# Optimization experiments

Measured on AMD Instinct MI355X. Metric: run time of the kernel, lower is better.

The kernel has to match this reference:

```python
import jax, jax.numpy as jnp
import numpy as np

D = 1024
H = 16
HD = D // H
B = 2
S = 2048


def setup_inputs() -> dict:
    key = jax.random.key(0)
    ks = jax.random.split(key, 9)
    sc = 1.0 / np.sqrt(D)
    return {
        "x": jax.random.normal(ks[0], (B, S, D), dtype=jnp.float32),
        "attention_mask": jnp.ones((B, S), dtype=jnp.int32),
        "Wq": jax.random.normal(ks[1], (D, D), dtype=jnp.float32) * sc,
        "bq": jax.random.normal(ks[2], (D,), dtype=jnp.float32) * 0.02,
        "Wk": jax.random.normal(ks[3], (D, D), dtype=jnp.float32) * sc,
        "bk": jax.random.normal(ks[4], (D,), dtype=jnp.float32) * 0.02,
        "Wv": jax.random.normal(ks[5], (D, D), dtype=jnp.float32) * sc,
        "bv": jax.random.normal(ks[6], (D,), dtype=jnp.float32) * 0.02,
        "Wo": jax.random.normal(ks[7], (D, D), dtype=jnp.float32) * sc,
        "bo": jax.random.normal(ks[8], (D,), dtype=jnp.float32) * 0.02,
    }


def reference(x, attention_mask, Wq, bq, Wk, bk, Wv, bv, Wo, bo):
    Bb, Ss, d = x.shape
    # projections (torch Linear: x @ W.T + b; here W stored as [in,out])
    q = (x @ Wq + bq).reshape(Bb, Ss, H, HD).transpose(0, 2, 1, 3)  # [B,H,S,hd]
    k = (x @ Wk + bk).reshape(Bb, Ss, H, HD).transpose(0, 2, 1, 3)
    v = (x @ Wv + bv).reshape(Bb, Ss, H, HD).transpose(0, 2, 1, 3)
    dots = jnp.einsum("bhqd,bhkd->bhqk", q, k) / np.sqrt(HD)  # [B,H,S,S]
    causal = jnp.triu(jnp.ones((Ss, Ss), dtype=bool), k=1)  # True above diagonal
    dots = jnp.where(causal[None, None], -jnp.inf, dots)
    pad = (attention_mask == 0)[:, None, None, :]  # [B,1,1,S]
    dots = jnp.where(pad, -jnp.inf, dots)
    scores = jax.nn.softmax(dots, axis=-1)
    o = jnp.einsum("bhqk,bhkd->bhqd", scores, v)  # [B,H,S,hd]
    o = o.transpose(0, 2, 1, 3).reshape(Bb, Ss, d)
    return o @ Wo + bo
```

## Files before the change

### kernel.cpp

```cpp
#include <hip/hip_runtime.h>

#define D_  1024
#define H_  16
#define HD_ 64
#define B_  2
#define S_  2048
#define M_  (B_*S_)

typedef _Float16 f16;
typedef _Float16 f16x8 __attribute__((ext_vector_type(8)));
typedef _Float16 f16x4 __attribute__((ext_vector_type(4)));
typedef _Float16 f16x2 __attribute__((ext_vector_type(2)));
typedef float    f32x4 __attribute__((ext_vector_type(4)));

#define GLOAD_LDS16(g, l) \
  __builtin_amdgcn_global_load_lds((__attribute__((address_space(1))) const void*)(g), \
                                   (__attribute__((address_space(3))) void*)(l), 16, 0, 0)

__global__ void k_cvt_x(const float* __restrict__ x, f16* __restrict__ xb) {
  int i = blockIdx.x * blockDim.x + threadIdx.x;
  float4 v = ((const float4*)x)[i];
  f16x4 o = { (f16)v.x, (f16)v.y, (f16)v.z, (f16)v.w };
  ((f16x4*)xb)[i] = o;
}

__global__ void k_twt(const float* __restrict__ W, f16* __restrict__ WT) {
  __shared__ float t[32][33];
  int n0 = blockIdx.x * 32, k0 = blockIdx.y * 32;
  int tx = threadIdx.x, ty = threadIdx.y;
  #pragma unroll
  for (int i = 0; i < 4; i++)
    t[ty + i*8][tx] = W[(size_t)(k0 + ty + i*8) * D_ + n0 + tx];
  __syncthreads();
  #pragma unroll
  for (int i = 0; i < 4; i++)
    WT[(size_t)(n0 + ty + i*8) * D_ + k0 + tx] = (f16)t[tx][ty + i*8];
}

template<int MODE>
__device__ __forceinline__ void gemm_body(const f16* __restrict__ A,
                                          const f16* __restrict__ Bt,
                                          const float* __restrict__ bias,
                                          void* __restrict__ Cout) {
  __shared__ __align__(16) f16 lA[128 * 32];
  __shared__ __align__(16) f16 lB[128 * 32];
  const int tid = threadIdx.x;
  const int wv = tid >> 6, lane = tid & 63;
  const int m0 = blockIdx.y * 128, n0 = blockIdx.x * 128;
  const int fr = lane & 15, fg = lane >> 4;
  const int wm = wv >> 1, wn = wv & 1;
  f32x4 acc[4][4] = {};

  for (int k0 = 0; k0 < D_; k0 += 32) {
    #pragma unroll
    for (int it = 0; it < 2; ++it) {
      int c = wv + it * 4;
      int row = c * 16 + (lane >> 2);
      int kk = (lane & 3) * 8;
      GLOAD_LDS16(A  + (size_t)(m0 + row) * D_ + k0 + kk, lA + c * 512);
      GLOAD_LDS16(Bt + (size_t)(n0 + row) * D_ + k0 + kk, lB + c * 512);
    }
    __syncthreads();
    f16x8 a[4], b[4];
    #pragma unroll
    for (int i = 0; i < 4; i++) a[i] = *(const f16x8*)&lA[(wm*64 + i*16 + fr) * 32 + fg * 8];
    #pragma unroll
    for (int j = 0; j < 4; j++) b[j] = *(const f16x8*)&lB[(wn*64 + j*16 + fr) * 32 + fg * 8];
    #pragma unroll
    for (int i = 0; i < 4; i++)
      #pragma unroll
      for (int j = 0; j < 4; j++)
        acc[i][j] = __builtin_amdgcn_mfma_f32_16x16x32_f16(a[i], b[j], acc[i][j], 0, 0, 0);
    __syncthreads();
  }

  #pragma unroll
  for (int i = 0; i < 4; i++) {
    #pragma unroll
    for (int j = 0; j < 4; j++) {
      int grow0 = m0 + wm*64 + i*16 + fg*4;
      int gcol  = n0 + wn*64 + j*16 + fr;
      float bb = bias[gcol];
      #pragma unroll
      for (int r = 0; r < 4; r++) {
        float val = acc[i][j][r] + bb;
        int grow = grow0 + r;
        if (MODE == 0) {
          int b = grow >> 11, s = grow & (S_ - 1);
          int h = gcol >> 6,  hd = gcol & (HD_ - 1);
          ((f16*)Cout)[((size_t)(b * H_ + h) * S_ + s) * HD_ + hd] = (f16)val;
        } else {
          ((float*)Cout)[(size_t)grow * D_ + gcol] = val;
        }
      }
    }
  }
}

__global__ __launch_bounds__(256) void k_gemm_qkv(const f16* __restrict__ A,
                                                  const f16* __restrict__ WT0,
                                                  const float* __restrict__ bq,
                                                  const float* __restrict__ bk,
                                                  const float* __restrict__ bv,
                                                  f16* __restrict__ qkv) {
  int z = blockIdx.z;
  const f16* Bt = WT0 + (size_t)z * D_ * D_;
  const float* bias = (z == 0) ? bq : (z == 1) ? bk : bv;
  f16* outp = qkv + (size_t)z * M_ * D_;
  gemm_body<0>(A, Bt, bias, outp);
}

__global__ __launch_bounds__(256) void k_gemm_out(const f16* __restrict__ A,
                                                  const f16* __restrict__ Bt,
                                                  const float* __restrict__ bias,
                                                  float* __restrict__ Cout) {
  gemm_body<1>(A, Bt, bias, Cout);
}

#define POFF 8.65617025f

__global__ __launch_bounds__(256) void k_attn(const f16* __restrict__ Qh,
                                              const f16* __restrict__ Kh,
                                              const f16* __restrict__ Vh,
                                              const int* __restrict__ am,
                                              f16* __restrict__ O) {
  __shared__ __align__(16) f16 kt[2][64 * 64];
  __shared__ __align__(16) f16 vt[2][64 * 64];
  __shared__ __align__(16) f16 pl[4][16 * 64];

  const int tid = threadIdx.x;
  const int wv = tid >> 6, lane = tid & 63;
  const int fr = lane & 15, fg = lane >> 4;

  const int d = blockIdx.x;
  const int x = d & 7, j = d >> 3;
  const int bh = x + 8 * (j & 3);
  const int slot = j >> 2;
  const int b = bh >> 4, h = bh & 15;

  const f16* Qb = Qh + (size_t)bh * S_ * HD_;
  const f16* Kb = Kh + (size_t)bh * S_ * HD_;
  const f16* Vb = Vh + (size_t)bh * S_ * HD_;
  const int* amb = am + b * S_;
  f16* plw = pl[wv];

  const f16 qs = (f16)0.18033688f;
  const int ksrc = 8 * ((lane & 7) ^ (lane >> 3));
  const int swz = (fr & 7) << 3;
  const int vkk = (tid >> 3) * 2, vd0 = (tid & 7) * 8;
  const int vswz2 = (tid & 3) << 4;
  const f32x4 cinit = { -POFF, -POFF, -POFF, -POFF };

#define STAGE_K(t_, c_) do { \
    const f16* kp_ = Kb + (size_t)((t_) * 64) * HD_; \
    GLOAD_LDS16(kp_ + (size_t)((wv*2+0)*8 + (lane >> 3)) * HD_ + ksrc, &kt[c_][(wv*2+0)*512]); \
    GLOAD_LDS16(kp_ + (size_t)((wv*2+1)*8 + (lane >> 3)) * HD_ + ksrc, &kt[c_][(wv*2+1)*512]); \
  } while (0)

#define LOAD_V(t_) do { \
    const f16* vp_ = Vb + (size_t)((t_) * 64 + vkk) * HD_ + vd0; \
    vA = *(const f16x8*)vp_; vBr = *(const f16x8*)(vp_ + HD_); \
  } while (0)

#define WRITE_V(c_) do { \
    _Pragma("unroll") \
    for (int j_ = 0; j_ < 8; ++j_) { \
      f16x2 pr_ = { vA[j_], vBr[j_] }; \
      *(f16x2*)&vt[c_][(vd0 + j_) * 64 + ((vkk ^ (j_ << 3)) ^ vswz2)] = pr_; \
    } \
  } while (0)

  f16x8 vA, vBr;

  auto run_tile = [&](int qt, int nkb) {
    const int q0w = qt * 64 + wv * 16;

    f16x8 qf0, qf1;
    {
      f16x8 r0 = *(const f16x8*)&Qb[(size_t)(q0w + fr) * HD_ + fg*8];
      f16x8 r1 = *(const f16x8*)&Qb[(size_t)(q0w + fr) * HD_ + 32 + fg*8];
      qf0 = r0 * qs; qf1 = r1 * qs;
    }

    f32x4 accO[4] = {};
    float lrl = 0.f;

    STAGE_K(0, 0);
    LOAD_V(0);
    WRITE_V(0);
    __syncthreads();

    int c = 0;
    for (int t = 0; t < nkb; ++t) {
      const int kb = t * 64;
      const bool pre = (t + 1 < nkb);
      if (pre) { STAGE_K(t + 1, c ^ 1); LOAD_V(t + 1); }

      int4 a4[4];
      #pragma unroll
      for (int tt = 0; tt < 4; ++tt) a4[tt] = *(const int4*)&amb[kb + tt*16 + fg*4];

      const int dq = q0w - kb;
      int tm = (dq + 15) >> 4; if (tm > 3) tm = 3;
      const bool fullb = (dq >= 63);

      f32x4 s[4];
      #pragma unroll
      for (int tt = 0; tt < 4; ++tt) s[tt] = cinit;

      __builtin_amdgcn_s_setprio(1);
      #pragma unroll
      for (int tt = 0; tt < 4; ++tt) {
        if (tt <= tm) {
          const int kr = (tt*16 + fr) * 64;
          f16x8 kf0 = *(const f16x8*)&kt[c][kr + ((     fg*8) ^ swz)];
          f16x8 kf1 = *(const f16x8*)&kt[c][kr + ((32 + fg*8) ^ swz)];
          s[tt] = __builtin_amdgcn_mfma_f32_16x16x32_f16(kf0, qf0, s[tt], 0, 0, 0);
          s[tt] = __builtin_amdgcn_mfma_f32_16x16x32_f16(kf1, qf1, s[tt], 0, 0, 0);
        }
      }
      __builtin_amdgcn_s_setprio(0);

      const int thr = dq + fr;
      #pragma unroll
      for (int tt = 0; tt < 4; ++tt) {
        f16x4 pk4 = {};
        if (tt <= tm) {
          #pragma unroll
          for (int r = 0; r < 4; ++r) {
            float sv = s[tt][r];
            if (!fullb) sv = (tt*16 + fg*4 + r <= thr) ? sv : -1e30f;
            float p = exp2f(sv);
            int mr_ = (r == 0) ? a4[tt].x : (r == 1) ? a4[tt].y : (r == 2) ? a4[tt].z : a4[tt].w;
            p = mr_ ? p : 0.0f;
            lrl += p;
            pk4[r] = (f16)p;
          }
        }
        *(f16x4*)&plw[fr * 64 + ((tt*16 + fg*4) ^ swz)] = pk4;
      }

      __builtin_amdgcn_s_setprio(1);
      #pragma unroll
      for (int ks = 0; ks < 2; ++ks) {
        if (ks <= (tm >> 1)) {
          f16x8 pa = *(const f16x8*)&plw[fr * 64 + ((ks*32 + fg*8) ^ swz)];
          #pragma unroll
          for (int nt = 0; nt < 4; ++nt) {
            f16x8 vf = *(const f16x8*)&vt[c][(nt*16 + fr) * 64 +
                         ((ks*32 + fg*8) ^ swz ^ (((2*nt + (fr >> 3)) & 3) << 4))];
            accO[nt] = __builtin_amdgcn_mfma_f32_16x16x32_f16(pa, vf, accO[nt], 0, 0, 0);
          }
        }
      }
      __builtin_amdgcn_s_setprio(0);

      if (pre) WRITE_V(c ^ 1);
      __syncthreads();
      c ^= 1;
    }

    float v = lrl;
    v += __shfl_xor(v, 16);
    v += __shfl_xor(v, 32);
    float inv[4];
    #pragma unroll
    for (int r = 0; r < 4; ++r) {
      float sum = __shfl(v, (lane & 48) + 4 * ((lane >> 4) & 3) + r);
      inv[r] = __builtin_amdgcn_rcpf(sum);
    }
    #pragma unroll
    for (int nt = 0; nt < 4; ++nt) {
      int col = h * HD_ + nt*16 + fr;
      #pragma unroll
      for (int r = 0; r < 4; ++r) {
        int row = q0w + fg*4 + r;
        O[((size_t)b * S_ + row) * D_ + col] = (f16)(accO[nt][r] * inv[r]);
      }
    }
  };

  run_tile(slot, slot + 1);
  run_tile(31 - slot, 32 - slot);

#undef STAGE_K
#undef LOAD_V
#undef WRITE_V
}

extern "C" void kernel_launch(void* const* d_in, const int* in_sizes, int n_in,
                              void* d_out, int out_size, void* d_ws, size_t ws_size,
                              hipStream_t stream) {
  const float* x  = (const float*)d_in[0];
  const int*   am = (const int*)d_in[1];
  const float* Wq = (const float*)d_in[2];
  const float* bq = (const float*)d_in[3];
  const float* Wk = (const float*)d_in[4];
  const float* bk = (const float*)d_in[5];
  const float* Wv = (const float*)d_in[6];
  const float* bv = (const float*)d_in[7];
  const float* Wo = (const float*)d_in[8];
  const float* bo = (const float*)d_in[9];

  char* ws = (char*)d_ws;
  f16* xb  = (f16*)(ws);
  f16* wt  = (f16*)(ws + (8u  << 20));
  f16* qkv = (f16*)(ws + (16u << 20));
  f16* Ob  = (f16*)(ws + (40u << 20));

  k_cvt_x<<<4096, 256, 0, stream>>>(x, xb);

  dim3 tb(32, 8), tg(32, 32);
  k_twt<<<tg, tb, 0, stream>>>(Wq, wt + 0 * (size_t)(D_ * D_));
  k_twt<<<tg, tb, 0, stream>>>(Wk, wt + 1 * (size_t)(D_ * D_));
  k_twt<<<tg, tb, 0, stream>>>(Wv, wt + 2 * (size_t)(D_ * D_));
  k_twt<<<tg, tb, 0, stream>>>(Wo, wt + 3 * (size_t)(D_ * D_));

  k_gemm_qkv<<<dim3(8, 32, 3), 256, 0, stream>>>(xb, wt, bq, bk, bv, qkv);

  k_attn<<<dim3(512), 256, 0, stream>>>(qkv,
                                        qkv + (size_t)M_ * D_,
                                        qkv + 2 * (size_t)M_ * D_,
                                        am, Ob);

  k_gemm_out<<<dim3(8, 32), 256, 0, stream>>>(Ob, wt + 3 * (size_t)(D_ * D_), bo,
                                              (float*)d_out);
}
```

Baseline: 138.7 us.

## Split attention KV range across two blocks and combine partials in separate kernel

The attention kernel now launches twice as many blocks. Each block covers half of the key range for its pair of query tiles and writes unnormalized partial outputs plus row sums to workspace buffers. A new combine kernel adds the two partials, normalizes them, and writes the head-interleaved layout consumed by the output GEMM. A block-level check of whether the whole padding mask is valid also skips the per-element mask loads and selects when no keys are masked. The goal is more parallelism and better load balance on the GPU, at the cost of an extra kernel launch, extra global traffic and aliased workspace reuse.

Measured after the change: 139.3 us. Within noise of the previous version (+0.4%).

```diff
diff --git a/kernel.cpp b/kernel.cpp
--- a/kernel.cpp
+++ b/kernel.cpp
@@ -123,7 +123,8 @@
                                               const f16* __restrict__ Kh,
                                               const f16* __restrict__ Vh,
                                               const int* __restrict__ am,
-                                              f16* __restrict__ O) {
+                                              f16* __restrict__ OpA, f16* __restrict__ OpB,
+                                              float* __restrict__ lpA, float* __restrict__ lpB) {
   __shared__ __align__(16) f16 kt[2][64 * 64];
   __shared__ __align__(16) f16 vt[2][64 * 64];
   __shared__ __align__(16) f16 pl[4][16 * 64];
@@ -133,16 +134,33 @@
   const int fr = lane & 15, fg = lane >> 4;
 
   const int d = blockIdx.x;
-  const int x = d & 7, j = d >> 3;
-  const int bh = x + 8 * (j & 3);
-  const int slot = j >> 2;
+  const int lo = d & 255, kk4 = d >> 8;
+  const int bh = lo & 31;
+  const int m  = (lo >> 5) + 8 * (kk4 & 1);
+  const int typeB = kk4 >> 1;
   const int b = bh >> 4, h = bh & 15;
+  (void)h;
+
+  f16*   Op = typeB ? OpB : OpA;
+  float* lp = typeB ? lpB : lpA;
 
   const f16* Qb = Qh + (size_t)bh * S_ * HD_;
   const f16* Kb = Kh + (size_t)bh * S_ * HD_;
   const f16* Vb = Vh + (size_t)bh * S_ * HD_;
   const int* amb = am + b * S_;
   f16* plw = pl[wv];
+
+  volatile int* flag = (volatile int*)&pl[0][0];
+  if (tid == 0) *flag = 1;
+  __syncthreads();
+  {
+    int mv = 1;
+    #pragma unroll
+    for (int i = 0; i < 8; ++i) mv &= amb[tid * 8 + i];
+    if (!mv) *flag = 0;
+  }
+  __syncthreads();
+  const bool allv = (*flag != 0);
 
   const f16 qs = (f16)0.18033688f;
   const int ksrc = 8 * ((lane & 7) ^ (lane >> 3));
@@ -172,120 +190,158 @@
 
   f16x8 vA, vBr;
 
-  auto run_tile = [&](int qt, int nkb) {
+  auto run_half = [&](int qt, int t0, int t1) {
     const int q0w = qt * 64 + wv * 16;
-
-    f16x8 qf0, qf1;
-    {
-      f16x8 r0 = *(const f16x8*)&Qb[(size_t)(q0w + fr) * HD_ + fg*8];
-      f16x8 r1 = *(const f16x8*)&Qb[(size_t)(q0w + fr) * HD_ + 32 + fg*8];
-      qf0 = r0 * qs; qf1 = r1 * qs;
-    }
-
     f32x4 accO[4] = {};
     float lrl = 0.f;
 
-    STAGE_K(0, 0);
-    LOAD_V(0);
-    WRITE_V(0);
-    __syncthreads();
-
-    int c = 0;
-    for (int t = 0; t < nkb; ++t) {
-      const int kb = t * 64;
-      const bool pre = (t + 1 < nkb);
-      if (pre) { STAGE_K(t + 1, c ^ 1); LOAD_V(t + 1); }
-
-      int4 a4[4];
-      #pragma unroll
-      for (int tt = 0; tt < 4; ++tt) a4[tt] = *(const int4*)&amb[kb + tt*16 + fg*4];
-
-      const int dq = q0w - kb;
-      int tm = (dq + 15) >> 4; if (tm > 3) tm = 3;
-      const bool fullb = (dq >= 63);
-
-      f32x4 s[4];
-      #pragma unroll
-      for (int tt = 0; tt < 4; ++tt) s[tt] = cinit;
-
-      __builtin_amdgcn_s_setprio(1);
-      #pragma unroll
-      for (int tt = 0; tt < 4; ++tt) {
-        if (tt <= tm) {
-          const int kr = (tt*16 + fr) * 64;
-          f16x8 kf0 = *(const f16x8*)&kt[c][kr + ((     fg*8) ^ swz)];
-          f16x8 kf1 = *(const f16x8*)&kt[c][kr + ((32 + fg*8) ^ swz)];
-          s[tt] = __builtin_amdgcn_mfma_f32_16x16x32_f16(kf0, qf0, s[tt], 0, 0, 0);
-          s[tt] = __builtin_amdgcn_mfma_f32_16x16x32_f16(kf1, qf1, s[tt], 0, 0, 0);
-        }
+    if (t0 < t1) {
+      f16x8 qf0, qf1;
+      {
+        f16x8 r0 = *(const f16x8*)&Qb[(size_t)(q0w + fr) * HD_ + fg*8];
+        f16x8 r1 = *(const f16x8*)&Qb[(size_t)(q0w + fr) * HD_ + 32 + fg*8];
+        qf0 = r0 * qs; qf1 = r1 * qs;
       }
-      __builtin_amdgcn_s_setprio(0);
-
-      const int thr = dq + fr;
-      #pragma unroll
-      for (int tt = 0; tt < 4; ++tt) {
-        f16x4 pk4 = {};
-        if (tt <= tm) {
-          #pragma unroll
-          for (int r = 0; r < 4; ++r) {
-            float sv = s[tt][r];
-            if (!fullb) sv = (tt*16 + fg*4 + r <= thr) ? sv : -1e30f;
-            float p = exp2f(sv);
-            int mr_ = (r == 0) ? a4[tt].x : (r == 1) ? a4[tt].y : (r == 2) ? a4[tt].z : a4[tt].w;
-            p = mr_ ? p : 0.0f;
-            lrl += p;
-            pk4[r] = (f16)p;
+
+      STAGE_K(t0, 0);
+      LOAD_V(t0);
+      WRITE_V(0);
+      __syncthreads();
+
+      int c = 0;
+      for (int t = t0; t < t1; ++t) {
+        const int kb = t * 64;
+        const bool pre = (t + 1 < t1);
+        if (pre) { STAGE_K(t + 1, c ^ 1); LOAD_V(t + 1); }
+
+        const int dq = q0w - kb;
+        int tm = (dq + 15) >> 4; if (tm > 3) tm = 3;
+        const bool fullb = (dq >= 63);
+
+        f32x4 s[4];
+        #pragma unroll
+        for (int tt = 0; tt < 4; ++tt) s[tt] = cinit;
+
+        __builtin_amdgcn_s_setprio(1);
+        #pragma unroll
+        for (int tt = 0; tt < 4; ++tt) {
+          if (tt <= tm) {
+            const int kr = (tt*16 + fr) * 64;
+            f16x8 kf0 = *(const f16x8*)&kt[c][kr + ((     fg*8) ^ swz)];
+            f16x8 kf1 = *(const f16x8*)&kt[c][kr + ((32 + fg*8) ^ swz)];
+            s[tt] = __builtin_amdgcn_mfma_f32_16x16x32_f16(kf0, qf0, s[tt], 0, 0, 0);
+            s[tt] = __builtin_amdgcn_mfma_f32_16x16x32_f16(kf1, qf1, s[tt], 0, 0, 0);
           }
         }
-        *(f16x4*)&plw[fr * 64 + ((tt*16 + fg*4) ^ swz)] = pk4;
-      }
-
-      __builtin_amdgcn_s_setprio(1);
-      #pragma unroll
-      for (int ks = 0; ks < 2; ++ks) {
-        if (ks <= (tm >> 1)) {
-          f16x8 pa = *(const f16x8*)&plw[fr * 64 + ((ks*32 + fg*8) ^ swz)];
+        __builtin_amdgcn_s_setprio(0);
+
+        const int thr = dq + fr;
+        if (allv) {
           #pragma unroll
-          for (int nt = 0; nt < 4; ++nt) {
-            f16x8 vf = *(const f16x8*)&vt[c][(nt*16 + fr) * 64 +
-                         ((ks*32 + fg*8) ^ swz ^ (((2*nt + (fr >> 3)) & 3) << 4))];
-            accO[nt] = __builtin_amdgcn_mfma_f32_16x16x32_f16(pa, vf, accO[nt], 0, 0, 0);
+          for (int tt = 0; tt < 4; ++tt) {
+            f16x4 pk4 = {};
+            if (tt <= tm) {
+              #pragma unroll
+              for (int r = 0; r < 4; ++r) {
+                float sv = s[tt][r];
+                if (!fullb) sv = (tt*16 + fg*4 + r <= thr) ? sv : -1e30f;
+                float p = exp2f(sv);
+                lrl += p;
+                pk4[r] = (f16)p;
+              }
+            }
+            *(f16x4*)&plw[fr * 64 + ((tt*16 + fg*4) ^ swz)] = pk4;
+          }
+        } else {
+          #pragma unroll
+          for (int tt = 0; tt < 4; ++tt) {
+            f16x4 pk4 = {};
+            if (tt <= tm) {
+              int4 a4 = *(const int4*)&amb[kb + tt*16 + fg*4];
+              #pragma unroll
+              for (int r = 0; r < 4; ++r) {
+                float sv = s[tt][r];
+                if (!fullb) sv = (tt*16 + fg*4 + r <= thr) ? sv : -1e30f;
+                float p = exp2f(sv);
+                int mr_ = (r == 0) ? a4.x : (r == 1) ? a4.y : (r == 2) ? a4.z : a4.w;
+                p = mr_ ? p : 0.0f;
+                lrl += p;
+                pk4[r] = (f16)p;
+              }
+            }
+            *(f16x4*)&plw[fr * 64 + ((tt*16 + fg*4) ^ swz)] = pk4;
           }
         }
+
+        __builtin_amdgcn_s_setprio(1);
+        #pragma unroll
+        for (int ks = 0; ks < 2; ++ks) {
+          if (ks <= (tm >> 1)) {
+            f16x8 pa = *(const f16x8*)&plw[fr * 64 + ((ks*32 + fg*8) ^ swz)];
+            #pragma unroll
+            for (int nt = 0; nt < 4; ++nt) {
+              f16x8 vf = *(const f16x8*)&vt[c][(nt*16 + fr) * 64 +
+                           ((ks*32 + fg*8) ^ swz ^ (((2*nt + (fr >> 3)) & 3) << 4))];
+              accO[nt] = __builtin_amdgcn_mfma_f32_16x16x32_f16(pa, vf, accO[nt], 0, 0, 0);
+            }
+          }
+        }
+        __builtin_amdgcn_s_setprio(0);
+
+        if (pre) WRITE_V(c ^ 1);
+        __syncthreads();
+        c ^= 1;
       }
-      __builtin_amdgcn_s_setprio(0);
-
-      if (pre) WRITE_V(c ^ 1);
-      __syncthreads();
-      c ^= 1;
     }
 
     float v = lrl;
     v += __shfl_xor(v, 16);
     v += __shfl_xor(v, 32);
-    float inv[4];
-    #pragma unroll
-    for (int r = 0; r < 4; ++r) {
-      float sum = __shfl(v, (lane & 48) + 4 * ((lane >> 4) & 3) + r);
-      inv[r] = __builtin_amdgcn_rcpf(sum);
-    }
+    if (lane < 16) lp[(size_t)bh * S_ + q0w + lane] = v;
+
+    f16* Oprow = Op + (size_t)bh * (S_ * HD_);
     #pragma unroll
     for (int nt = 0; nt < 4; ++nt) {
-      int col = h * HD_ + nt*16 + fr;
+      int col = nt*16 + fr;
       #pragma unroll
       for (int r = 0; r < 4; ++r) {
         int row = q0w + fg*4 + r;
-        O[((size_t)b * S_ + row) * D_ + col] = (f16)(accO[nt][r] * inv[r]);
+        Oprow[(size_t)row * HD_ + col] = (f16)accO[nt][r];
       }
     }
   };
 
-  run_tile(slot, slot + 1);
-  run_tile(31 - slot, 32 - slot);
+  const int haM = (m + 2) >> 1;
+  const int haC = (33 - m) >> 1;
+  if (!typeB) {
+    run_half(m,      0,   haM);
+    run_half(31 - m, 0,   haC);
+  } else {
+    run_half(m,      haM, m + 1);
+    run_half(31 - m, haC, 32 - m);
+  }
 
 #undef STAGE_K
 #undef LOAD_V
 #undef WRITE_V
+}
+
+__global__ __launch_bounds__(256) void k_comb(const f16* __restrict__ OA,
+                                              const f16* __restrict__ OB,
+                                              const float* __restrict__ lA,
+                                              const float* __restrict__ lB,
+                                              f16* __restrict__ Obf) {
+  int gid = blockIdx.x * 256 + threadIdx.x;
+  int seg = gid & 7, rowg = gid >> 3;
+  int bh = rowg >> 11, row = rowg & 2047;
+  f16x8 a  = ((const f16x8*)OA)[gid];
+  f16x8 b2 = ((const f16x8*)OB)[gid];
+  float inv = __builtin_amdgcn_rcpf(lA[rowg] + lB[rowg]);
+  f16x8 o;
+  #pragma unroll
+  for (int j = 0; j < 8; ++j) o[j] = (f16)(((float)a[j] + (float)b2[j]) * inv);
+  int bb = bh >> 4, hh = bh & 15;
+  *(f16x8*)&Obf[((size_t)(bb * S_ + row)) * D_ + hh * 64 + seg * 8] = o;
 }
 
 extern "C" void kernel_launch(void* const* d_in, const int* in_sizes, int n_in,
@@ -303,10 +359,14 @@
   const float* bo = (const float*)d_in[9];
 
   char* ws = (char*)d_ws;
-  f16* xb  = (f16*)(ws);
-  f16* wt  = (f16*)(ws + (8u  << 20));
-  f16* qkv = (f16*)(ws + (16u << 20));
-  f16* Ob  = (f16*)(ws + (40u << 20));
+  f16*   xb  = (f16*)(ws);
+  f16*   wt  = (f16*)(ws + (8u  << 20));
+  f16*   qkv = (f16*)(ws + (16u << 20));
+  f16*   OpA = (f16*)(ws + (40u << 20));
+  f16*   OpB = xb;
+  float* lpA = (float*)(ws + (8u << 20));
+  float* lpB = (float*)(ws + (8u << 20) + (256u << 10));
+  f16*   Obf = qkv;
 
   k_cvt_x<<<4096, 256, 0, stream>>>(x, xb);
 
@@ -318,11 +378,13 @@
 
   k_gemm_qkv<<<dim3(8, 32, 3), 256, 0, stream>>>(xb, wt, bq, bk, bv, qkv);
 
-  k_attn<<<dim3(512), 256, 0, stream>>>(qkv,
-                                        qkv + (size_t)M_ * D_,
-                                        qkv + 2 * (size_t)M_ * D_,
-                                        am, Ob);
-
-  k_gemm_out<<<dim3(8, 32), 256, 0, stream>>>(Ob, wt + 3 * (size_t)(D_ * D_), bo,
+  k_attn<<<dim3(1024), 256, 0, stream>>>(qkv,
+                                         qkv + (size_t)M_ * D_,
+                                         qkv + 2 * (size_t)M_ * D_,
+                                         am, OpA, OpB, lpA, lpB);
+
+  k_comb<<<dim3(2048), 256, 0, stream>>>(OpA, OpB, lpA, lpB, Obf);
+
+  k_gemm_out<<<dim3(8, 32), 256, 0, stream>>>(Obf, wt + 3 * (size_t)(D_ * D_), bo,
                                               (float*)d_out);
 }
```
